# Kernel tuning notes

Hardware: AMD Instinct MI355X
Metric: run time of the kernel (lower is better)

The kernel has to match this reference:

```python
import jax, jax.numpy as jnp
import numpy as np
from jax import lax

NFFT = 1024
STRIDE = 256
CUTOFF = NFFT // 2 + 1  # 513


def make_basis():
    # DFT matrix rows (real then imag parts up to Nyquist), windowed by periodic Hann.
    fft = np.fft.fft(np.eye(NFFT))
    basis = np.concatenate([np.real(fft)[:CUTOFF], np.imag(fft)[:CUTOFF]], axis=0)
    n = np.arange(NFFT)
    hann = 0.5 - 0.5 * np.cos(2.0 * np.pi * n / NFFT)  # scipy get_window('hann', N) periodic
    return jnp.asarray((hann * basis).astype(np.float32))[:, None, :]  # [2*CUTOFF, 1, NFFT]


def setup_inputs() -> dict:
    key = jax.random.key(0)
    x = jax.random.normal(key, (32, 1, 262144), dtype=jnp.float32)
    basis = make_basis()
    return {"x": x, "basis": basis}


def reference(x, basis):
    # conv1d(1 -> 2*CUTOFF, kernel=NFFT, stride=STRIDE, padding=NFFT, no bias)
    spec = lax.conv_general_dilated(
        x, basis,
        window_strides=(STRIDE,),
        padding=[(NFFT, NFFT)],
        dimension_numbers=("NCH", "OIH", "NCH"),
    )  # [B, 2*CUTOFF, F]
    real = spec[:, :CUTOFF]
    imag = spec[:, CUTOFF:]
    mag = jnp.sqrt(real * real + imag * imag)
    angle = jnp.arctan2(imag, real)
    return (mag, angle)
```

## Files before the change

### kernel.cpp

```cpp
#include <hip/hip_runtime.h>
#include <hip/hip_fp16.h>
#include <math.h>


#define NFFT     1024
#define STRIDE_  256
#define CUTOFF_  513
#define NFRAMES  1029
#define BATCH_   32
#define XLEN     262144
#define FB       16
#define TPB      512
#define NTILES   65
#define RSTRIDE  (FB + 1)
#define RESSZ    8800
#define QCAP     256
#define TAU      0.05f
#define PI_F     3.14159265358979323846f
#define PIH_F    1.57079632679489661923f
#define TWO_PI   6.28318530717958647692f

__device__ __forceinline__ int ridx(int f, int tt) {
    return f * RSTRIDE + ((f >> 4) << 1) + tt;
}

__device__ __forceinline__ float fast_atan2(float y, float x) {
    float ax = fabsf(x), ay = fabsf(y);
    float mx = fmaxf(ax, ay), mn = fminf(ax, ay);
    float a  = mn * __builtin_amdgcn_rcpf(mx);
    float s  = a * a;
    float r  = a * (0.9998660f + s * (-0.3302995f + s * (0.1801410f + s * (-0.0851330f))));
    if (ay > ax) r = PIH_F - r;
    if (x < 0.0f) r = PI_F - r;
    return copysignf(r, y);
}

#define XSTAGE(DIST, TC, TS) do {                        \
    float br_ = __shfl_xor(ar, DIST, 64);                \
    float bi_ = __shfl_xor(ai, DIST, 64);                \
    float dr_ = (lane & DIST) ? (br_ - ar) : (ar + br_); \
    float di_ = (lane & DIST) ? (bi_ - ai) : (ai + bi_); \
    ar = dr_ * (TC) - di_ * (TS);                        \
    ai = dr_ * (TS) + di_ * (TC);                        \
} while (0)

__global__ __launch_bounds__(TPB, 4) void stft_fft_kernel(
    const float* __restrict__ x, const float* __restrict__ basis,
    float* __restrict__ out)
{
    __shared__ __half resM[RESSZ];
    __shared__ __half resA[RESSZ];
    __shared__ unsigned queue[QCAP];
    __shared__ int qn;

    const int tid  = threadIdx.x;
    const int wave = tid >> 6;
    const int lane = tid & 63;
    const int bx   = blockIdx.x;
    const int n    = bx / NTILES;
    const int tile = bx % NTILES;
    const int t0   = tile * FB;
    const int nt   = min(FB, NFRAMES - t0);
    const float* __restrict__ xb = x + (size_t)n * XLEN;

    if (tid == 0) qn = 0;
    const int K1     = __brev((unsigned)lane) >> 26;
    const int p0lane = __brev((unsigned)((64 - K1) & 63)) >> 26;
    __syncthreads();

    const int fa = 2 * wave;
    if (fa < nt) {
        const int fbv   = fa + 1;
        const bool hasB = (fbv < nt);
        const int baseA = (t0 + fa) * STRIDE_ - NFFT;
        const bool zeroA = (baseA + NFFT <= 0) || (baseA >= XLEN);

        if (zeroA && !hasB) {
            #pragma unroll
            for (int k2 = 0; k2 < 16; ++k2) {
                const int f = k2 + 16 * K1;
                if (f <= NFFT / 2) {
                    resM[ridx(f, fa)] = __float2half(0.0f);
                    resA[ridx(f, fa)] = __float2half(0.0f);
                }
            }
        } else {
            float sl, cl;
            sincosf(TWO_PI * (float)lane * (1.0f / 1024.0f), &sl, &cl);

            float raw[20];
            #pragma unroll
            for (int r = 0; r < 20; ++r) {
                const int pa = baseA + lane + 64 * r;
                raw[r] = (pa >= 0 && pa < XLEN) ? xb[pa] : 0.0f;
            }

            constexpr float WC[16] = {
                1.f,  0.92387953251128676f,  0.70710678118654752f,  0.38268343236508977f,
                0.f, -0.38268343236508977f, -0.70710678118654752f, -0.92387953251128676f,
               -1.f, -0.92387953251128676f, -0.70710678118654752f, -0.38268343236508977f,
                0.f,  0.38268343236508977f,  0.70710678118654752f,  0.92387953251128676f };
            constexpr float WS[16] = {
                0.f,  0.38268343236508977f,  0.70710678118654752f,  0.92387953251128676f,
                1.f,  0.92387953251128676f,  0.70710678118654752f,  0.38268343236508977f,
                0.f, -0.38268343236508977f, -0.70710678118654752f, -0.92387953251128676f,
               -1.f, -0.92387953251128676f, -0.70710678118654752f, -0.38268343236508977f };
            const float hb = hasB ? 1.0f : 0.0f;
            float yr[16], yi[16];
            #pragma unroll
            for (int r = 0; r < 16; ++r) {
                const float w = 0.5f - 0.5f * (cl * WC[r] - sl * WS[r]);
                yr[r] = raw[r] * w;
                yi[r] = raw[r + 4] * w * hb;
            }

            float Ar[16], Ai[16];
            #pragma unroll
            for (int r0 = 0; r0 < 4; ++r0) {
                float q0r = yr[r0],      q0i = yi[r0];
                float q1r = yr[r0 + 4],  q1i = yi[r0 + 4];
                float q2r = yr[r0 + 8],  q2i = yi[r0 + 8];
                float q3r = yr[r0 + 12], q3i = yi[r0 + 12];
                float t0r = q0r + q2r, t0i = q0i + q2i;
                float t1r = q0r - q2r, t1i = q0i - q2i;
                float t2r = q1r + q3r, t2i = q1i + q3i;
                float t3r = q1i - q3i, t3i = q3r - q1r;
                Ar[4*r0+0] = t0r + t2r; Ai[4*r0+0] = t0i + t2i;
                Ar[4*r0+1] = t1r + t3r; Ai[4*r0+1] = t1i + t3i;
                Ar[4*r0+2] = t0r - t2r; Ai[4*r0+2] = t0i - t2i;
                Ar[4*r0+3] = t1r - t3r; Ai[4*r0+3] = t1i - t3i;
            }
            constexpr float TWC[16] = {
                1.f, 1.f, 1.f, 1.f,
                1.f,  0.92387953251128676f,  0.70710678118654752f,  0.38268343236508977f,
                1.f,  0.70710678118654752f,  0.f,                  -0.70710678118654752f,
                1.f,  0.38268343236508977f, -0.70710678118654752f, -0.92387953251128676f };
            constexpr float TWS[16] = {
                0.f, 0.f, 0.f, 0.f,
                0.f, -0.38268343236508977f, -0.70710678118654752f, -0.92387953251128676f,
                0.f, -0.70710678118654752f, -1.f,                  -0.70710678118654752f,
                0.f, -0.92387953251128676f, -0.70710678118654752f,  0.38268343236508977f };
            #pragma unroll
            for (int idx = 0; idx < 16; ++idx) {
                float tr = Ar[idx] * TWC[idx] - Ai[idx] * TWS[idx];
                Ai[idx]  = Ar[idx] * TWS[idx] + Ai[idx] * TWC[idx];
                Ar[idx]  = tr;
            }
            #pragma unroll
            for (int m = 0; m < 4; ++m) {
                float q0r = Ar[m],      q0i = Ai[m];
                float q1r = Ar[4 + m],  q1i = Ai[4 + m];
                float q2r = Ar[8 + m],  q2i = Ai[8 + m];
                float q3r = Ar[12 + m], q3i = Ai[12 + m];
                float t0r = q0r + q2r, t0i = q0i + q2i;
                float t1r = q0r - q2r, t1i = q0i - q2i;
                float t2r = q1r + q3r, t2i = q1i + q3i;
                float t3r = q1i - q3i, t3i = q3r - q1r;
                yr[m + 0]  = t0r + t2r; yi[m + 0]  = t0i + t2i;
                yr[m + 4]  = t1r + t3r; yi[m + 4]  = t1i + t3i;
                yr[m + 8]  = t0r - t2r; yi[m + 8]  = t0i - t2i;
                yr[m + 12] = t1r - t3r; yi[m + 12] = t1i - t3i;
            }

            {
                const float c1 = cl, s1 = -sl;
                float cc = 1.0f, ssv = 0.0f;
                #pragma unroll
                for (int k2 = 0; k2 < 16; ++k2) {
                    float tr = yr[k2] * cc - yi[k2] * ssv;
                    yi[k2]   = yr[k2] * ssv + yi[k2] * cc;
                    yr[k2]   = tr;
                    float nc = cc * c1 - ssv * s1;
                    ssv = cc * s1 + ssv * c1;
                    cc = nc;
                }
            }

            float tc32, ts32; __sincosf(-TWO_PI * (float)(lane & 31) * (1.0f/64.0f), &ts32, &tc32);
            if (!(lane & 32)) { tc32 = 1.0f; ts32 = 0.0f; }
            float tc16, ts16; __sincosf(-TWO_PI * (float)(lane & 15) * (1.0f/32.0f), &ts16, &tc16);
            if (!(lane & 16)) { tc16 = 1.0f; ts16 = 0.0f; }
            float tc8, ts8;   __sincosf(-TWO_PI * (float)(lane & 7)  * (1.0f/16.0f), &ts8,  &tc8);
            if (!(lane & 8))  { tc8 = 1.0f; ts8 = 0.0f; }
            float tc4, ts4;   __sincosf(-TWO_PI * (float)(lane & 3)  * (1.0f/8.0f),  &ts4,  &tc4);
            if (!(lane & 4))  { tc4 = 1.0f; ts4 = 0.0f; }
            float tc2 = 1.0f, ts2 = 0.0f;
            if ((lane & 2) && (lane & 1)) { tc2 = 0.0f; ts2 = -1.0f; }

            #pragma unroll
            for (int k2 = 0; k2 < 16; ++k2) {
                float ar = yr[k2], ai = yi[k2];
                XSTAGE(32, tc32, ts32);
                XSTAGE(16, tc16, ts16);
                XSTAGE(8,  tc8,  ts8);
                XSTAGE(4,  tc4,  ts4);
                XSTAGE(2,  tc2,  ts2);
                {
                    float br_ = __shfl_xor(ar, 1, 64);
                    float bi_ = __shfl_xor(ai, 1, 64);
                    float dr_ = (lane & 1) ? (br_ - ar) : (ar + br_);
                    float di_ = (lane & 1) ? (bi_ - ai) : (ai + bi_);
                    ar = dr_; ai = di_;
                }
                yr[k2] = ar; yi[k2] = ai;
            }

            #pragma unroll
            for (int k2 = 0; k2 < 16; ++k2) {
                float prr, pii;
                if (k2 == 0) {
                    prr = __shfl(yr[0], p0lane, 64);
                    pii = __shfl(yi[0], p0lane, 64);
                } else {
                    prr = __shfl_xor(yr[16 - k2], 63, 64);
                    pii = __shfl_xor(yi[16 - k2], 63, 64);
                }
                const int f = k2 + 16 * K1;
                if (f <= NFFT / 2) {
                    const float R0 = yr[k2], I0 = yi[k2];
                    if (zeroA) {
                        resM[ridx(f, fa)] = __float2half(0.0f);
                        resA[ridx(f, fa)] = __float2half(0.0f);
                    } else {
                        float reA = 0.5f * (R0 + prr), imA = 0.5f * (I0 - pii);
                        resM[ridx(f, fa)] = __float2half(sqrtf(reA * reA + imA * imA));
                        resA[ridx(f, fa)] = __float2half(fast_atan2(imA, reA));
                        if (fabsf(imA) < TAU && reA < TAU) {
                            int qi = atomicAdd(&qn, 1);
                            if (qi < QCAP)
                                queue[qi] = ((unsigned)fa << 16) | (unsigned)f;
                        }
                    }
                    if (hasB) {
                        float reB = 0.5f * (I0 + pii), imB = 0.5f * (prr - R0);
                        resM[ridx(f, fbv)] = __float2half(sqrtf(reB * reB + imB * imB));
                        resA[ridx(f, fbv)] = __float2half(fast_atan2(imB, reB));
                        if (fabsf(imB) < TAU && reB < TAU) {
                            int qi = atomicAdd(&qn, 1);
                            if (qi < QCAP)
                                queue[qi] = ((unsigned)fbv << 16) | (unsigned)f;
                        }
                    }
                }
            }
        }
    }
    __syncthreads();

    {
        const int nq = min(qn, QCAP);
        for (int qi = wave; qi < nq; qi += TPB / 64) {
            unsigned e = queue[qi];
            int f  = (int)(e & 0xffffu);
            int ft = (int)(e >> 16);
            int base = (t0 + ft) * STRIDE_ - NFFT;
            const float* __restrict__ br = basis + (size_t)f * NFFT;
            const float* __restrict__ bi = basis + (size_t)(CUTOFF_ + f) * NFFT;
            double sr0 = 0.0, si0 = 0.0, sr1 = 0.0, si1 = 0.0;
            #pragma unroll 2
            for (int hh = lane; hh < NFFT; hh += 128) {
                int p0 = base + hh;
                int p1 = p0 + 64;
                if (p0 >= 0 && p0 < XLEN) {
                    double xv = (double)xb[p0];
                    sr0 += xv * (double)br[hh];
                    si0 += xv * (double)bi[hh];
                }
                if (p1 >= 0 && p1 < XLEN) {
                    double xv = (double)xb[p1];
                    sr1 += xv * (double)br[hh + 64];
                    si1 += xv * (double)bi[hh + 64];
                }
            }
            double sr = sr0 + sr1, si = si0 + si1;
            #pragma unroll
            for (int off = 32; off; off >>= 1) {
                sr += __shfl_down(sr, off);
                si += __shfl_down(si, off);
            }
            if (lane == 0) {
                float re = (float)sr, im = (float)si;
                resM[ridx(f, ft)] = __float2half(sqrtf(re * re + im * im));
                resA[ridx(f, ft)] = __float2half(atan2f(im, re));
            }
        }
    }
    __syncthreads();

    const size_t magbase = (size_t)n * CUTOFF_ * NFRAMES;
    const size_t angoff  = (size_t)BATCH_ * CUTOFF_ * NFRAMES;
    for (int idx = tid; idx < CUTOFF_ * FB; idx += TPB) {
        int f  = idx >> 4;
        int tt = idx & (FB - 1);
        if (tt < nt) {
            size_t o = magbase + (size_t)f * NFRAMES + (size_t)(t0 + tt);
            out[o]          = __half2float(resM[ridx(f, tt)]);
            out[angoff + o] = __half2float(resA[ridx(f, tt)]);
        }
    }
}

extern "C" void kernel_launch(void* const* d_in, const int* in_sizes, int n_in,
                              void* d_out, int out_size, void* d_ws, size_t ws_size,
                              hipStream_t stream) {
    const float* x     = (const float*)d_in[0];
    const float* basis = (const float*)d_in[1];
    float* out = (float*)d_out;
    dim3 grid(BATCH_ * NTILES);
    dim3 block(TPB);
    stft_fft_kernel<<<grid, block, 0, stream>>>(x, basis, out);
}
```

Before: 332.7 us.

## Process two frame pairs per wave and halve the block size

```diff
diff --git a/kernel.cpp b/kernel.cpp
--- a/kernel.cpp
+++ b/kernel.cpp
@@ -10,7 +10,7 @@
 #define BATCH_   32
 #define XLEN     262144
 #define FB       16
-#define TPB      512
+#define TPB      256
 #define NTILES   65
 #define RSTRIDE  (FB + 1)
 #define RESSZ    8800
@@ -44,7 +44,7 @@
     ai = dr_ * (TS) + di_ * (TC);                        \
 } while (0)
 
-__global__ __launch_bounds__(TPB, 4) void stft_fft_kernel(
+__global__ __launch_bounds__(TPB, 3) void stft_fft_kernel(
     const float* __restrict__ x, const float* __restrict__ basis,
     float* __restrict__ out)
 {
@@ -68,59 +68,72 @@
     const int p0lane = __brev((unsigned)((64 - K1) & 63)) >> 26;
     __syncthreads();
 
-    const int fa = 2 * wave;
-    if (fa < nt) {
-        const int fbv   = fa + 1;
-        const bool hasB = (fbv < nt);
-        const int baseA = (t0 + fa) * STRIDE_ - NFFT;
-        const bool zeroA = (baseA + NFFT <= 0) || (baseA >= XLEN);
-
-        if (zeroA && !hasB) {
-            #pragma unroll
-            for (int k2 = 0; k2 < 16; ++k2) {
-                const int f = k2 + 16 * K1;
-                if (f <= NFFT / 2) {
-                    resM[ridx(f, fa)] = __float2half(0.0f);
-                    resA[ridx(f, fa)] = __float2half(0.0f);
-                }
-            }
-        } else {
-            float sl, cl;
-            sincosf(TWO_PI * (float)lane * (1.0f / 1024.0f), &sl, &cl);
-
-            float raw[20];
-            #pragma unroll
-            for (int r = 0; r < 20; ++r) {
-                const int pa = baseA + lane + 64 * r;
-                raw[r] = (pa >= 0 && pa < XLEN) ? xb[pa] : 0.0f;
-            }
-
-            constexpr float WC[16] = {
-                1.f,  0.92387953251128676f,  0.70710678118654752f,  0.38268343236508977f,
-                0.f, -0.38268343236508977f, -0.70710678118654752f, -0.92387953251128676f,
-               -1.f, -0.92387953251128676f, -0.70710678118654752f, -0.38268343236508977f,
-                0.f,  0.38268343236508977f,  0.70710678118654752f,  0.92387953251128676f };
-            constexpr float WS[16] = {
-                0.f,  0.38268343236508977f,  0.70710678118654752f,  0.92387953251128676f,
-                1.f,  0.92387953251128676f,  0.70710678118654752f,  0.38268343236508977f,
-                0.f, -0.38268343236508977f, -0.70710678118654752f, -0.92387953251128676f,
-               -1.f, -0.92387953251128676f, -0.70710678118654752f, -0.38268343236508977f };
-            const float hb = hasB ? 1.0f : 0.0f;
-            float yr[16], yi[16];
+    const int fa0 = 4 * wave;
+    if (fa0 < nt) {
+        int  fa[2];   fa[0] = fa0;  fa[1] = fa0 + 2;
+        bool ex[2], hasB[2], zero[2];
+        int  base[2];
+        #pragma unroll
+        for (int p = 0; p < 2; ++p) {
+            ex[p]   = (fa[p] < nt);
+            hasB[p] = (fa[p] + 1 < nt);
+            base[p] = (t0 + fa[p]) * STRIDE_ - NFFT;
+            zero[p] = (base[p] + NFFT <= 0) || (base[p] >= XLEN);
+        }
+
+        float sl, cl;
+        sincosf(TWO_PI * (float)lane * (1.0f / 1024.0f), &sl, &cl);
+
+        const int base0 = base[0];
+        float raw[28];
+        #pragma unroll
+        for (int r = 0; r < 28; ++r) {
+            const int pa = base0 + lane + 64 * r;
+            raw[r] = (pa >= 0 && pa < XLEN) ? xb[pa] : 0.0f;
+        }
+
+        constexpr float WC[16] = {
+            1.f,  0.92387953251128676f,  0.70710678118654752f,  0.38268343236508977f,
+            0.f, -0.38268343236508977f, -0.70710678118654752f, -0.92387953251128676f,
+           -1.f, -0.92387953251128676f, -0.70710678118654752f, -0.38268343236508977f,
+            0.f,  0.38268343236508977f,  0.70710678118654752f,  0.92387953251128676f };
+        constexpr float WS[16] = {
+            0.f,  0.38268343236508977f,  0.70710678118654752f,  0.92387953251128676f,
+            1.f,  0.92387953251128676f,  0.70710678118654752f,  0.38268343236508977f,
+            0.f, -0.38268343236508977f, -0.70710678118654752f, -0.92387953251128676f,
+           -1.f, -0.92387953251128676f, -0.70710678118654752f, -0.38268343236508977f };
+
+        float yr[2][16], yi[2][16];
+        #pragma unroll
+        for (int p = 0; p < 2; ++p) {
+            const float hb = hasB[p] ? 1.0f : 0.0f;
             #pragma unroll
             for (int r = 0; r < 16; ++r) {
                 const float w = 0.5f - 0.5f * (cl * WC[r] - sl * WS[r]);
-                yr[r] = raw[r] * w;
-                yi[r] = raw[r + 4] * w * hb;
-            }
-
+                yr[p][r] = raw[8 * p + r] * w;
+                yi[p][r] = raw[8 * p + r + 4] * w * hb;
+            }
+        }
+
+        constexpr float TWC[16] = {
+            1.f, 1.f, 1.f, 1.f,
+            1.f,  0.92387953251128676f,  0.70710678118654752f,  0.38268343236508977f,
+            1.f,  0.70710678118654752f,  0.f,                  -0.70710678118654752f,
+            1.f,  0.38268343236508977f, -0.70710678118654752f, -0.92387953251128676f };
+        constexpr float TWS[16] = {
+            0.f, 0.f, 0.f, 0.f,
+            0.f, -0.38268343236508977f, -0.70710678118654752f, -0.92387953251128676f,
+            0.f, -0.70710678118654752f, -1.f,                  -0.70710678118654752f,
+            0.f, -0.92387953251128676f, -0.70710678118654752f,  0.38268343236508977f };
+        #pragma unroll
+        for (int p = 0; p < 2; ++p) {
             float Ar[16], Ai[16];
             #pragma unroll
             for (int r0 = 0; r0 < 4; ++r0) {
-                float q0r = yr[r0],      q0i = yi[r0];
-                float q1r = yr[r0 + 4],  q1i = yi[r0 + 4];
-                float q2r = yr[r0 + 8],  q2i = yi[r0 + 8];
-                float q3r = yr[r0 + 12], q3i = yi[r0 + 12];
+                float q0r = yr[p][r0],      q0i = yi[p][r0];
+                float q1r = yr[p][r0 + 4],  q1i = yi[p][r0 + 4];
+                float q2r = yr[p][r0 + 8],  q2i = yi[p][r0 + 8];
+                float q3r = yr[p][r0 + 12], q3i = yi[p][r0 + 12];
                 float t0r = q0r + q2r, t0i = q0i + q2i;
                 float t1r = q0r - q2r, t1i = q0i - q2i;
                 float t2r = q1r + q3r, t2i = q1i + q3i;
@@ -130,16 +143,6 @@
                 Ar[4*r0+2] = t0r - t2r; Ai[4*r0+2] = t0i - t2i;
                 Ar[4*r0+3] = t1r - t3r; Ai[4*r0+3] = t1i - t3i;
             }
-            constexpr float TWC[16] = {
-                1.f, 1.f, 1.f, 1.f,
-                1.f,  0.92387953251128676f,  0.70710678118654752f,  0.38268343236508977f,
-                1.f,  0.70710678118654752f,  0.f,                  -0.70710678118654752f,
-                1.f,  0.38268343236508977f, -0.70710678118654752f, -0.92387953251128676f };
-            constexpr float TWS[16] = {
-                0.f, 0.f, 0.f, 0.f,
-                0.f, -0.38268343236508977f, -0.70710678118654752f, -0.92387953251128676f,
-                0.f, -0.70710678118654752f, -1.f,                  -0.70710678118654752f,
-                0.f, -0.92387953251128676f, -0.70710678118654752f,  0.38268343236508977f };
             #pragma unroll
             for (int idx = 0; idx < 16; ++idx) {
                 float tr = Ar[idx] * TWC[idx] - Ai[idx] * TWS[idx];
@@ -156,40 +159,46 @@
                 float t1r = q0r - q2r, t1i = q0i - q2i;
                 float t2r = q1r + q3r, t2i = q1i + q3i;
                 float t3r = q1i - q3i, t3i = q3r - q1r;
-                yr[m + 0]  = t0r + t2r; yi[m + 0]  = t0i + t2i;
-                yr[m + 4]  = t1r + t3r; yi[m + 4]  = t1i + t3i;
-                yr[m + 8]  = t0r - t2r; yi[m + 8]  = t0i - t2i;
-                yr[m + 12] = t1r - t3r; yi[m + 12] = t1i - t3i;
-            }
-
-            {
-                const float c1 = cl, s1 = -sl;
-                float cc = 1.0f, ssv = 0.0f;
+                yr[p][m + 0]  = t0r + t2r; yi[p][m + 0]  = t0i + t2i;
+                yr[p][m + 4]  = t1r + t3r; yi[p][m + 4]  = t1i + t3i;
+                yr[p][m + 8]  = t0r - t2r; yi[p][m + 8]  = t0i - t2i;
+                yr[p][m + 12] = t1r - t3r; yi[p][m + 12] = t1i - t3i;
+            }
+        }
+
+        {
+            const float c1 = cl, s1 = -sl;
+            float cc = 1.0f, ssv = 0.0f;
+            #pragma unroll
+            for (int k2 = 0; k2 < 16; ++k2) {
                 #pragma unroll
-                for (int k2 = 0; k2 < 16; ++k2) {
-                    float tr = yr[k2] * cc - yi[k2] * ssv;
-                    yi[k2]   = yr[k2] * ssv + yi[k2] * cc;
-                    yr[k2]   = tr;
-                    float nc = cc * c1 - ssv * s1;
-                    ssv = cc * s1 + ssv * c1;
-                    cc = nc;
-                }
-            }
-
-            float tc32, ts32; __sincosf(-TWO_PI * (float)(lane & 31) * (1.0f/64.0f), &ts32, &tc32);
-            if (!(lane & 32)) { tc32 = 1.0f; ts32 = 0.0f; }
-            float tc16, ts16; __sincosf(-TWO_PI * (float)(lane & 15) * (1.0f/32.0f), &ts16, &tc16);
-            if (!(lane & 16)) { tc16 = 1.0f; ts16 = 0.0f; }
-            float tc8, ts8;   __sincosf(-TWO_PI * (float)(lane & 7)  * (1.0f/16.0f), &ts8,  &tc8);
-            if (!(lane & 8))  { tc8 = 1.0f; ts8 = 0.0f; }
-            float tc4, ts4;   __sincosf(-TWO_PI * (float)(lane & 3)  * (1.0f/8.0f),  &ts4,  &tc4);
-            if (!(lane & 4))  { tc4 = 1.0f; ts4 = 0.0f; }
-            float tc2 = 1.0f, ts2 = 0.0f;
-            if ((lane & 2) && (lane & 1)) { tc2 = 0.0f; ts2 = -1.0f; }
-
-            #pragma unroll
-            for (int k2 = 0; k2 < 16; ++k2) {
-                float ar = yr[k2], ai = yi[k2];
+                for (int p = 0; p < 2; ++p) {
+                    float tr  = yr[p][k2] * cc - yi[p][k2] * ssv;
+                    yi[p][k2] = yr[p][k2] * ssv + yi[p][k2] * cc;
+                    yr[p][k2] = tr;
+                }
+                float nc = cc * c1 - ssv * s1;
+                ssv = cc * s1 + ssv * c1;
+                cc = nc;
+            }
+        }
+
+        float tc32, ts32; __sincosf(-TWO_PI * (float)(lane & 31) * (1.0f/64.0f), &ts32, &tc32);
+        if (!(lane & 32)) { tc32 = 1.0f; ts32 = 0.0f; }
+        float tc16, ts16; __sincosf(-TWO_PI * (float)(lane & 15) * (1.0f/32.0f), &ts16, &tc16);
+        if (!(lane & 16)) { tc16 = 1.0f; ts16 = 0.0f; }
+        float tc8, ts8;   __sincosf(-TWO_PI * (float)(lane & 7)  * (1.0f/16.0f), &ts8,  &tc8);
+        if (!(lane & 8))  { tc8 = 1.0f; ts8 = 0.0f; }
+        float tc4, ts4;   __sincosf(-TWO_PI * (float)(lane & 3)  * (1.0f/8.0f),  &ts4,  &tc4);
+        if (!(lane & 4))  { tc4 = 1.0f; ts4 = 0.0f; }
+        float tc2 = 1.0f, ts2 = 0.0f;
+        if ((lane & 2) && (lane & 1)) { tc2 = 0.0f; ts2 = -1.0f; }
+
+        #pragma unroll
+        for (int k2 = 0; k2 < 16; ++k2) {
+            #pragma unroll
+            for (int p = 0; p < 2; ++p) {
+                float ar = yr[p][k2], ai = yi[p][k2];
                 XSTAGE(32, tc32, ts32);
                 XSTAGE(16, tc16, ts16);
                 XSTAGE(8,  tc8,  ts8);
@@ -202,43 +211,48 @@
                     float di_ = (lane & 1) ? (bi_ - ai) : (ai + bi_);
                     ar = dr_; ai = di_;
                 }
-                yr[k2] = ar; yi[k2] = ai;
-            }
-
+                yr[p][k2] = ar; yi[p][k2] = ai;
+            }
+        }
+
+        #pragma unroll
+        for (int p = 0; p < 2; ++p) {
+            if (!ex[p]) continue;
+            const int faP = fa[p], fbP = faP + 1;
             #pragma unroll
             for (int k2 = 0; k2 < 16; ++k2) {
                 float prr, pii;
                 if (k2 == 0) {
-                    prr = __shfl(yr[0], p0lane, 64);
-                    pii = __shfl(yi[0], p0lane, 64);
+                    prr = __shfl(yr[p][0], p0lane, 64);
+                    pii = __shfl(yi[p][0], p0lane, 64);
                 } else {
-                    prr = __shfl_xor(yr[16 - k2], 63, 64);
-                    pii = __shfl_xor(yi[16 - k2], 63, 64);
+                    prr = __shfl_xor(yr[p][16 - k2], 63, 64);
+                    pii = __shfl_xor(yi[p][16 - k2], 63, 64);
                 }
                 const int f = k2 + 16 * K1;
                 if (f <= NFFT / 2) {
-                    const float R0 = yr[k2], I0 = yi[k2];
-                    if (zeroA) {
-                        resM[ridx(f, fa)] = __float2half(0.0f);
-                        resA[ridx(f, fa)] = __float2half(0.0f);
+                    const float R0 = yr[p][k2], I0 = yi[p][k2];
+                    if (zero[p]) {
+                        resM[ridx(f, faP)] = __float2half(0.0f);
+                        resA[ridx(f, faP)] = __float2half(0.0f);
                     } else {
                         float reA = 0.5f * (R0 + prr), imA = 0.5f * (I0 - pii);
-                        resM[ridx(f, fa)] = __float2half(sqrtf(reA * reA + imA * imA));
-                        resA[ridx(f, fa)] = __float2half(fast_atan2(imA, reA));
+                        resM[ridx(f, faP)] = __float2half(sqrtf(reA * reA + imA * imA));
+                        resA[ridx(f, faP)] = __float2half(fast_atan2(imA, reA));
                         if (fabsf(imA) < TAU && reA < TAU) {
                             int qi = atomicAdd(&qn, 1);
                             if (qi < QCAP)
-                                queue[qi] = ((unsigned)fa << 16) | (unsigned)f;
+                                queue[qi] = ((unsigned)faP << 16) | (unsigned)f;
                         }
                     }
-                    if (hasB) {
+                    if (hasB[p]) {
                         float reB = 0.5f * (I0 + pii), imB = 0.5f * (prr - R0);
-                        resM[ridx(f, fbv)] = __float2half(sqrtf(reB * reB + imB * imB));
-                        resA[ridx(f, fbv)] = __float2half(fast_atan2(imB, reB));
+                        resM[ridx(f, fbP)] = __float2half(sqrtf(reB * reB + imB * imB));
+                        resA[ridx(f, fbP)] = __float2half(fast_atan2(imB, reB));
                         if (fabsf(imB) < TAU && reB < TAU) {
                             int qi = atomicAdd(&qn, 1);
                             if (qi < QCAP)
-                                queue[qi] = ((unsigned)fbv << 16) | (unsigned)f;
+                                queue[qi] = ((unsigned)fbP << 16) | (unsigned)f;
                         }
                     }
                 }
```

New measurement: 382.5 us. 15.0% more time.
